# Optimization experiments

Measured on AMD Instinct MI355X. Metric: run time of the kernel, lower is better.

Reference implementation:

```python
import jax, jax.numpy as jnp
import numpy as np

N = 50000      # nodes
E = 800000     # edges (avg degree 16)
CIN = 64       # in_channels
COUT = 128     # hidden_channels (block out_channels)
TC = 512       # time_channels = 4*hidden
H = 4          # attention heads
DH = COUT // H # head dim
G = 8          # group-norm groups
SLOPE = 0.01   # LeakyReLU default slope


def group_norm(x, w, b, groups=G, eps=1e-5):
    n, c = x.shape
    xg = x.reshape(n, groups, c // groups)
    mu = xg.mean(-1, keepdims=True)
    var = xg.var(-1, keepdims=True)
    xn = ((xg - mu) * jax.lax.rsqrt(var + eps)).reshape(n, c)
    return xn * w + b


def gcn_conv(x, W, b, row, col, ew, n):
    # GCNConv: add self loops (weight 1), symmetric normalization
    sl = jnp.arange(n)
    r = jnp.concatenate([row, sl])
    c = jnp.concatenate([col, sl])
    w2 = jnp.concatenate([ew, jnp.ones((n,), ew.dtype)])
    deg = jax.ops.segment_sum(w2, c, num_segments=n)
    dinv = jnp.where(deg > 0, jax.lax.rsqrt(deg), 0.0)
    norm = dinv[r] * w2 * dinv[c]            # [E+N]
    xw = x @ W                                # [N, Cout]
    out = jax.ops.segment_sum(norm[:, None] * xw[r], c, num_segments=n)
    return out + b


def gat_conv(x, Wa, a_src, a_dst, a_edge, ba, row, col, ew, n):
    # GAT-style attention conv; self-loop edge weight filled with max(edge_weight)
    sl = jnp.arange(n)
    fill = ew.max()
    r = jnp.concatenate([row, sl])
    c = jnp.concatenate([col, sl])
    w2 = jnp.concatenate([ew, jnp.full((n,), fill, ew.dtype)])
    h = (x @ Wa).reshape(n, H, DH)            # [N, H, DH]
    al_s = (h * a_src).sum(-1)                # [N, H]
    al_d = (h * a_dst).sum(-1)                # [N, H]
    logits = jax.nn.leaky_relu(al_s[r] + al_d[c] + a_edge * w2[:, None], 0.2)
    m = jax.ops.segment_max(logits, c, num_segments=n)
    e = jnp.exp(logits - m[c])
    s = jax.ops.segment_sum(e, c, num_segments=n)
    alpha = e / (s[c] + 1e-16)                # [E+N, H]
    out = jax.ops.segment_sum(alpha[:, :, None] * h[r], c, num_segments=n)
    return out.reshape(n, H * DH) + ba


def setup_inputs() -> dict:
    key = jax.random.key(0)
    ks = jax.random.split(key, 24)
    def w(k, shape, fan_in):
        return (jax.random.normal(k, shape, jnp.float32) / np.sqrt(fan_in)).astype(jnp.float32)
    inp = {
        "x": jax.random.normal(ks[0], (N, CIN), jnp.float32),
        "t": jax.random.normal(ks[1], (TC,), jnp.float32),
        "edge_index": jax.random.randint(ks[2], (2, E), 0, N, jnp.int32),
        "edge_weight": jax.random.uniform(ks[3], (E,), jnp.float32),
        # ResBlock norm/conv params
        "gn0_w": jnp.ones((CIN,), jnp.float32), "gn0_b": jnp.zeros((CIN,), jnp.float32),
        "W1": w(ks[4], (CIN, COUT), CIN), "b1": jnp.zeros((COUT,), jnp.float32),
        "gn1_w": jnp.ones((COUT,), jnp.float32), "gn1_b": jnp.zeros((COUT,), jnp.float32),
        "W2": w(ks[5], (COUT, COUT), COUT), "b2": jnp.zeros((COUT,), jnp.float32),
        "Wres": w(ks[6], (CIN, COUT), CIN),
        "te_w": w(ks[7], (TC, COUT), TC), "te_b": jnp.zeros((COUT,), jnp.float32),
        # AttnBlock params
        "gn2_w": jnp.ones((COUT,), jnp.float32), "gn2_b": jnp.zeros((COUT,), jnp.float32),
        "Wa": w(ks[8], (COUT, H * DH), COUT),
        "a_src": w(ks[9], (H, DH), DH), "a_dst": w(ks[10], (H, DH), DH),
        "a_edge": w(ks[11], (H,), 1), "ba": jnp.zeros((H * DH,), jnp.float32),
    }
    return inp


def reference(x, t, edge_index, edge_weight,
              gn0_w, gn0_b, W1, b1, gn1_w, gn1_b, W2, b2, Wres, te_w, te_b,
              gn2_w, gn2_b, Wa, a_src, a_dst, a_edge, ba):
    row, col = edge_index[0], edge_index[1]
    leaky = lambda z: jax.nn.leaky_relu(z, SLOPE)
    # ResBlock (n_layers=2)
    h = gcn_conv(leaky(group_norm(x, gn0_w, gn0_b)), W1, b1, row, col, edge_weight, N)
    tt = leaky(t) @ te_w + te_b               # time embed, broadcasts over nodes
    h = h + tt
    h = gcn_conv(leaky(group_norm(h, gn1_w, gn1_b)), W2, b2, row, col, edge_weight, N)
    h = h + x @ Wres                          # residual (Cin != Cout -> Linear)
    # AttnBlock (n_layers=1)
    a = leaky(group_norm(h, gn2_w, gn2_b))
    out = gat_conv(a, Wa, a_src, a_dst, a_edge, ba, row, col, edge_weight, N)
    return out
```

## Files before the change

### kernel.cpp

```cpp
#include <hip/hip_runtime.h>
#include <math.h>

#define ELLW 48
#define FB 4

typedef __attribute__((ext_vector_type(8))) short frag_ab;
typedef __attribute__((ext_vector_type(4))) float frag_cd;

__device__ __forceinline__ float lk(float v, float s) { return v > 0.f ? v : v * s; }
__device__ __forceinline__ unsigned short f2b(float f) {
    unsigned u = __float_as_uint(f);
    return (unsigned short)((u + 0x7fffu + ((u >> 16) & 1u)) >> 16);
}
__device__ __forceinline__ float b2f(unsigned h) { return __uint_as_float(h << 16); }

__global__ __launch_bounds__(256) void k_init(int* cnt, float* tt,
                                              const float* __restrict__ te_b,
                                              const float* __restrict__ b1, int n) {
    int i = blockIdx.x * 256 + threadIdx.x;
    if (i < n) cnt[i] = 0;
    if (i < 128) tt[i] = te_b[i] + b1[i];
}

__global__ __launch_bounds__(256) void k_fill_ell(const int* __restrict__ row,
                                                  const int* __restrict__ col,
                                                  const float* __restrict__ ew,
                                                  int* cnt, unsigned* __restrict__ ell,
                                                  float* __restrict__ bmax, int E) {
    int base = blockIdx.x * (256 * FB);
    int tid = threadIdx.x;
    int r[FB], c[FB]; float w[FB]; bool v[FB];
#pragma unroll
    for (int i = 0; i < FB; ++i) {
        int e = base + i * 256 + tid;
        v[i] = (e < E);
        r[i] = 0; c[i] = 0; w[i] = 0.f;
        if (v[i]) { r[i] = row[e]; c[i] = col[e]; w[i] = ew[e]; }
    }
    int pos[FB];
#pragma unroll
    for (int i = 0; i < FB; ++i)
        if (v[i]) pos[i] = atomicAdd(&cnt[c[i]], 1);
#pragma unroll
    for (int i = 0; i < FB; ++i)
        if (v[i] && pos[i] < ELLW)
            ell[(size_t)c[i] * ELLW + pos[i]] = (unsigned)r[i] | ((unsigned)f2b(w[i]) << 16);
    float m = 0.f;
#pragma unroll
    for (int i = 0; i < FB; ++i) m = fmaxf(m, w[i]);
    for (int o = 32; o; o >>= 1) m = fmaxf(m, __shfl_down(m, o, 64));
    __shared__ float sm[4];
    if ((tid & 63) == 0) sm[tid >> 6] = m;
    __syncthreads();
    if (tid == 0) bmax[blockIdx.x] = fmaxf(fmaxf(sm[0], sm[1]), fmaxf(sm[2], sm[3]));
}

__global__ __launch_bounds__(256) void k_node_deg(const int* __restrict__ cnt,
                                                  const unsigned* __restrict__ ell,
                                                  float* __restrict__ dinv,
                                                  const float* __restrict__ bmax,
                                                  float* __restrict__ fill, int n, int nb) {
    int tid = threadIdx.x;
    int i = blockIdx.x * 256 + tid;
    if (i < n) {
        int c = min(cnt[i], ELLW);
        const unsigned* p = ell + (size_t)i * ELLW;
        float s = 1.f;
        for (int j = 0; j < c; ++j) s += b2f(p[j] >> 16);
        dinv[i] = rsqrtf(s);
    }
    if (blockIdx.x == 0) {
        float m = 0.f;
        for (int k = tid; k < nb; k += 256) m = fmaxf(m, bmax[k]);
        for (int o = 32; o; o >>= 1) m = fmaxf(m, __shfl_down(m, o, 64));
        __shared__ float sm[4];
        if ((tid & 63) == 0) sm[tid >> 6] = m;
        __syncthreads();
        if (tid == 0) *fill = fmaxf(fmaxf(sm[0], sm[1]), fmaxf(sm[2], sm[3]));
    }
}

__global__ __launch_bounds__(128) void k_tt(const float* __restrict__ t,
                                            const float* __restrict__ te_w, float* tt) {
    int co = threadIdx.x;
    int k0 = blockIdx.x * 32;
    float s = 0.f;
    for (int k = k0; k < k0 + 32; ++k) {
        float tv = t[k]; tv = tv > 0.f ? tv : 0.01f * tv;
        s = fmaf(tv, te_w[k * 128 + co], s);
    }
    unsafeAtomicAdd(&tt[co], s);
}

template <int K>
__device__ __forceinline__ void repack1(const float* __restrict__ W,
                                        unsigned short* __restrict__ Wp, int i) {
    int k = i >> 7, nn = i & 127;
    int kc = k >> 5, quad = (k >> 3) & 3, j = k & 7;
    Wp[(((size_t)(kc * 4 + quad) * 128) + nn) * 8 + j] = f2b(W[i]);
}

__global__ __launch_bounds__(256) void k_repack_all(const float* __restrict__ W1,
                                                    const float* __restrict__ W2,
                                                    const float* __restrict__ Wa,
                                                    const float* __restrict__ Wres,
                                                    unsigned short* W1p, unsigned short* W2p,
                                                    unsigned short* Wap, unsigned short* Wrp) {
    int i = blockIdx.x * 256 + threadIdx.x;
    if (i < 8192)        repack1<64>(W1, W1p, i);
    else if (i < 24576)  repack1<128>(W2, W2p, i - 8192);
    else if (i < 40960)  repack1<128>(Wa, Wap, i - 24576);
    else if (i < 49152)  repack1<64>(Wres, Wrp, i - 40960);
}

template <int C>
__global__ __launch_bounds__(256) void k_gn(const float* __restrict__ in,
                                            const float* __restrict__ gw,
                                            const float* __restrict__ gb,
                                            unsigned short* __restrict__ outh,
                                            unsigned short* __restrict__ rawh, int n) {
    constexpr int CPG = C / 8;
    int gid = blockIdx.x * 256 + threadIdx.x;
    int row = gid >> 3, g = gid & 7;
    if (row >= n) return;
    const float* p = in + (size_t)row * C + g * CPG;
    float v[CPG];
#pragma unroll
    for (int j = 0; j < CPG; j += 4) {
        float4 t4 = *(const float4*)(p + j);
        v[j] = t4.x; v[j + 1] = t4.y; v[j + 2] = t4.z; v[j + 3] = t4.w;
    }
    float s = 0.f, s2 = 0.f;
#pragma unroll
    for (int j = 0; j < CPG; ++j) { s += v[j]; s2 += v[j] * v[j]; }
    float mu = s * (1.0f / CPG);
    float var = s2 * (1.0f / CPG) - mu * mu;
    float rstd = rsqrtf(var + 1e-5f);
    const float* wj = gw + g * CPG;
    const float* bj = gb + g * CPG;
    unsigned pk[CPG / 2];
#pragma unroll
    for (int j = 0; j < CPG; j += 2) {
        float y0 = lk((v[j + 0] - mu) * rstd * wj[j + 0] + bj[j + 0], 0.01f);
        float y1 = lk((v[j + 1] - mu) * rstd * wj[j + 1] + bj[j + 1], 0.01f);
        pk[j / 2] = (unsigned)f2b(y0) | ((unsigned)f2b(y1) << 16);
    }
    unsigned* q = (unsigned*)(outh + (size_t)row * C + g * CPG);
#pragma unroll
    for (int j = 0; j < CPG / 2; j += 4) *(uint4*)(q + j) = *(uint4*)(pk + j);
    if (rawh) {
#pragma unroll
        for (int j = 0; j < CPG; j += 2)
            pk[j / 2] = (unsigned)f2b(v[j]) | ((unsigned)f2b(v[j + 1]) << 16);
        unsigned* q2 = (unsigned*)(rawh + (size_t)row * C + g * CPG);
#pragma unroll
        for (int j = 0; j < CPG / 2; j += 4) *(uint4*)(q2 + j) = *(uint4*)(pk + j);
    }
}

template <int K, int SCALE>
__global__ __launch_bounds__(256) void k_mgemm(const unsigned short* __restrict__ Xh,
                                               const unsigned short* __restrict__ Wp,
                                               unsigned short* __restrict__ OUTh,
                                               const float* __restrict__ dinv, int n) {
    int tid = threadIdx.x;
    int wave = tid >> 6, lane = tid & 63;
    int quad = lane >> 4, l16 = lane & 15;
    int rbase = blockIdx.x * 64 + wave * 16;
    int arow = rbase + l16; if (arow >= n) arow = n - 1;
    frag_cd acc[8];
#pragma unroll
    for (int t = 0; t < 8; ++t) acc[t] = (frag_cd){0.f, 0.f, 0.f, 0.f};
    const unsigned short* ap = Xh + (size_t)arow * K + quad * 8;
#pragma unroll
    for (int kc = 0; kc < K / 32; ++kc) {
        frag_ab a = *(const frag_ab*)(ap + kc * 32);
        const unsigned short* bp = Wp + ((size_t)(kc * 4 + quad) * 128 + l16) * 8;
#pragma unroll
        for (int t = 0; t < 8; ++t) {
            frag_ab b = *(const frag_ab*)(bp + (size_t)t * 128);
            acc[t] = __builtin_amdgcn_mfma_f32_16x16x32_bf16(a, b, acc[t], 0, 0, 0);
        }
    }
#pragma unroll
    for (int reg = 0; reg < 4; ++reg) {
        int r = rbase + quad * 4 + reg;
        if (r >= n) continue;
        float sc = 1.f;
        if constexpr (SCALE) sc = dinv[r];
#pragma unroll
        for (int t = 0; t < 8; ++t)
            OUTh[(size_t)r * 128 + t * 16 + l16] = f2b(sc * acc[t][reg]);
    }
}

__global__ __launch_bounds__(256) void k_mgemm2(const unsigned short* __restrict__ X1,
                                                const unsigned short* __restrict__ W2p,
                                                const unsigned short* __restrict__ X2,
                                                const unsigned short* __restrict__ Wrp,
                                                unsigned short* __restrict__ OUTh,
                                                float* __restrict__ C2,
                                                const float* __restrict__ bias,
                                                const float* __restrict__ dinv, int n) {
    int tid = threadIdx.x;
    int wave = tid >> 6, lane = tid & 63;
    int quad = lane >> 4, l16 = lane & 15;
    int rbase = blockIdx.x * 64 + wave * 16;
    int arow = rbase + l16; if (arow >= n) arow = n - 1;
    frag_cd acc1[8], acc2[8];
#pragma unroll
    for (int t = 0; t < 8; ++t) {
        acc1[t] = (frag_cd){0.f, 0.f, 0.f, 0.f};
        acc2[t] = (frag_cd){0.f, 0.f, 0.f, 0.f};
    }
    const unsigned short* ap1 = X1 + (size_t)arow * 128 + quad * 8;
#pragma unroll
    for (int kc = 0; kc < 4; ++kc) {
        frag_ab a = *(const frag_ab*)(ap1 + kc * 32);
        const unsigned short* bp = W2p + ((size_t)(kc * 4 + quad) * 128 + l16) * 8;
#pragma unroll
        for (int t = 0; t < 8; ++t) {
            frag_ab b = *(const frag_ab*)(bp + (size_t)t * 128);
            acc1[t] = __builtin_amdgcn_mfma_f32_16x16x32_bf16(a, b, acc1[t], 0, 0, 0);
        }
    }
    const unsigned short* ap2 = X2 + (size_t)arow * 64 + quad * 8;
#pragma unroll
    for (int kc = 0; kc < 2; ++kc) {
        frag_ab a = *(const frag_ab*)(ap2 + kc * 32);
        const unsigned short* bp = Wrp + ((size_t)(kc * 4 + quad) * 128 + l16) * 8;
#pragma unroll
        for (int t = 0; t < 8; ++t) {
            frag_ab b = *(const frag_ab*)(bp + (size_t)t * 128);
            acc2[t] = __builtin_amdgcn_mfma_f32_16x16x32_bf16(a, b, acc2[t], 0, 0, 0);
        }
    }
#pragma unroll
    for (int reg = 0; reg < 4; ++reg) {
        int r = rbase + quad * 4 + reg;
        if (r >= n) continue;
        float sc = dinv[r];
#pragma unroll
        for (int t = 0; t < 8; ++t) {
            int c = t * 16 + l16;
            size_t o = (size_t)r * 128 + c;
            OUTh[o] = f2b(sc * acc1[t][reg]);
            C2[o] = bias[c] + acc2[t][reg];
        }
    }
}

template <int BASEVEC>
__global__ __launch_bounds__(256) void k_gather_gn(const int* __restrict__ cnt,
                                                   const unsigned* __restrict__ ell,
                                                   const float* __restrict__ dinv,
                                                   const unsigned short* __restrict__ Bh,
                                                   const float* __restrict__ basevec,
                                                   const float* __restrict__ basebuf,
                                                   const float* __restrict__ gw,
                                                   const float* __restrict__ gb,
                                                   unsigned short* __restrict__ outh, int n) {
    int gid = blockIdx.x * 256 + threadIdx.x;
    int node = gid >> 5, q = gid & 31;
    if (node >= n) return;
    int s = node * ELLW;
    int e2 = s + min(cnt[node], ELLW);
    float a0 = 0.f, a1 = 0.f, a2 = 0.f, a3 = 0.f;
    int j = s;
    for (; j + 4 <= e2; j += 4) {
        uint4 pe = *(const uint4*)(ell + j);
        int r0 = pe.x & 0xffffu, r1 = pe.y & 0xffffu, r2 = pe.z & 0xffffu, r3 = pe.w & 0xffffu;
        float w0 = b2f(pe.x >> 16), w1 = b2f(pe.y >> 16);
        float w2 = b2f(pe.z >> 16), w3 = b2f(pe.w >> 16);
        uint2 v0 = *(const uint2*)(Bh + (size_t)r0 * 128 + q * 4);
        uint2 v1 = *(const uint2*)(Bh + (size_t)r1 * 128 + q * 4);
        uint2 v2 = *(const uint2*)(Bh + (size_t)r2 * 128 + q * 4);
        uint2 v3 = *(const uint2*)(Bh + (size_t)r3 * 128 + q * 4);
        a0 = fmaf(w0, b2f(v0.x & 0xffffu), a0); a1 = fmaf(w0, b2f(v0.x >> 16), a1);
        a2 = fmaf(w0, b2f(v0.y & 0xffffu), a2); a3 = fmaf(w0, b2f(v0.y >> 16), a3);
        a0 = fmaf(w1, b2f(v1.x & 0xffffu), a0); a1 = fmaf(w1, b2f(v1.x >> 16), a1);
        a2 = fmaf(w1, b2f(v1.y & 0xffffu), a2); a3 = fmaf(w1, b2f(v1.y >> 16), a3);
        a0 = fmaf(w2, b2f(v2.x & 0xffffu), a0); a1 = fmaf(w2, b2f(v2.x >> 16), a1);
        a2 = fmaf(w2, b2f(v2.y & 0xffffu), a2); a3 = fmaf(w2, b2f(v2.y >> 16), a3);
        a0 = fmaf(w3, b2f(v3.x & 0xffffu), a0); a1 = fmaf(w3, b2f(v3.x >> 16), a1);
        a2 = fmaf(w3, b2f(v3.y & 0xffffu), a2); a3 = fmaf(w3, b2f(v3.y >> 16), a3);
    }
    for (; j < e2; ++j) {
        unsigned pe = ell[j];
        int r = pe & 0xffffu;
        float nw = b2f(pe >> 16);
        uint2 hv = *(const uint2*)(Bh + (size_t)r * 128 + q * 4);
        a0 = fmaf(nw, b2f(hv.x & 0xffffu), a0);
        a1 = fmaf(nw, b2f(hv.x >> 16), a1);
        a2 = fmaf(nw, b2f(hv.y & 0xffffu), a2);
        a3 = fmaf(nw, b2f(hv.y >> 16), a3);
    }
    float dc = dinv[node];
    uint2 sv = *(const uint2*)(Bh + (size_t)node * 128 + q * 4);
    a0 = dc * (a0 + b2f(sv.x & 0xffffu));
    a1 = dc * (a1 + b2f(sv.x >> 16));
    a2 = dc * (a2 + b2f(sv.y & 0xffffu));
    a3 = dc * (a3 + b2f(sv.y >> 16));
    float h0, h1, h2, h3;
    if constexpr (BASEVEC) {
        float4 bb = *(const float4*)(basevec + q * 4);
        h0 = bb.x + a0; h1 = bb.y + a1; h2 = bb.z + a2; h3 = bb.w + a3;
    } else {
        float4 bb = *(const float4*)(basebuf + (size_t)node * 128 + q * 4);
        h0 = bb.x + a0; h1 = bb.y + a1; h2 = bb.z + a2; h3 = bb.w + a3;
    }
    float sum = (h0 + h1) + (h2 + h3);
    float sq = fmaf(h0, h0, fmaf(h1, h1, fmaf(h2, h2, h3 * h3)));
    sum += __shfl_xor(sum, 1, 64); sum += __shfl_xor(sum, 2, 64);
    sq  += __shfl_xor(sq, 1, 64);  sq  += __shfl_xor(sq, 2, 64);
    float mu = sum * (1.0f / 16.0f);
    float var = sq * (1.0f / 16.0f) - mu * mu;
    float rstd = rsqrtf(var + 1e-5f);
    float4 gwv = *(const float4*)(gw + q * 4);
    float4 gbv = *(const float4*)(gb + q * 4);
    float y0 = lk((h0 - mu) * rstd * gwv.x + gbv.x, 0.01f);
    float y1 = lk((h1 - mu) * rstd * gwv.y + gbv.y, 0.01f);
    float y2 = lk((h2 - mu) * rstd * gwv.z + gbv.z, 0.01f);
    float y3 = lk((h3 - mu) * rstd * gwv.w + gbv.w, 0.01f);
    uint2 o;
    o.x = (unsigned)f2b(y0) | ((unsigned)f2b(y1) << 16);
    o.y = (unsigned)f2b(y2) | ((unsigned)f2b(y3) << 16);
    *(uint2*)(outh + (size_t)node * 128 + q * 4) = o;
}

__global__ __launch_bounds__(256) void k_al(const unsigned short* __restrict__ HAh,
                                            const float* __restrict__ a_src,
                                            const float* __restrict__ a_dst,
                                            float* __restrict__ als, float* __restrict__ ald, int n) {
    int gid = blockIdx.x * 256 + threadIdx.x;
    if (gid >= n * 4) return;
    int row = gid >> 2, hd = gid & 3;
    const unsigned* p = (const unsigned*)(HAh + (size_t)row * 128 + hd * 32);
    float ss = 0.f, sd = 0.f;
#pragma unroll
    for (int j = 0; j < 16; ++j) {
        unsigned u = p[j];
        float f0 = b2f(u & 0xffffu), f1 = b2f(u >> 16);
        float s0 = a_src[hd * 32 + j * 2], s1 = a_src[hd * 32 + j * 2 + 1];
        float d0 = a_dst[hd * 32 + j * 2], d1 = a_dst[hd * 32 + j * 2 + 1];
        ss = fmaf(f0, s0, fmaf(f1, s1, ss));
        sd = fmaf(f0, d0, fmaf(f1, d1, sd));
    }
    als[gid] = ss; ald[gid] = sd;
}

__global__ __launch_bounds__(256) void k_gat_gather(const int* __restrict__ cnt,
                                                    const unsigned* __restrict__ ell,
                                                    const float* __restrict__ als,
                                                    const float* __restrict__ ald,
                                                    const float* __restrict__ a_edge,
                                                    const float* __restrict__ fill,
                                                    const unsigned short* __restrict__ HAh,
                                                    const float* __restrict__ ba,
                                                    float* __restrict__ out, int n) {
    int gid = blockIdx.x * 256 + threadIdx.x;
    int node = gid >> 5, q = gid & 31, hd = q >> 3;
    if (node >= n) return;
    int s = node * ELLW;
    int e2 = s + min(cnt[node], ELLW);
    float ae = a_edge[hd];
    float aldc = ald[node * 4 + hd];
    float wself = *fill;
    float pself = __expf(lk(als[node * 4 + hd] + aldc + ae * wself, 0.2f));
    float den = pself;
    uint2 hv = *(const uint2*)(HAh + (size_t)node * 128 + q * 4);
    float a0 = pself * b2f(hv.x & 0xffffu), a1 = pself * b2f(hv.x >> 16);
    float a2 = pself * b2f(hv.y & 0xffffu), a3 = pself * b2f(hv.y >> 16);
    int j = s;
    for (; j + 4 <= e2; j += 4) {
        uint4 pe = *(const uint4*)(ell + j);
        int r0 = pe.x & 0xffffu, r1 = pe.y & 0xffffu, r2 = pe.z & 0xffffu, r3 = pe.w & 0xffffu;
        float w0 = b2f(pe.x >> 16), w1 = b2f(pe.y >> 16);
        float w2 = b2f(pe.z >> 16), w3 = b2f(pe.w >> 16);
        float s0 = als[r0 * 4 + hd], s1 = als[r1 * 4 + hd];
        float s2 = als[r2 * 4 + hd], s3 = als[r3 * 4 + hd];
        uint2 v0 = *(const uint2*)(HAh + (size_t)r0 * 128 + q * 4);
        uint2 v1 = *(const uint2*)(HAh + (size_t)r1 * 128 + q * 4);
        uint2 v2 = *(const uint2*)(HAh + (size_t)r2 * 128 + q * 4);
        uint2 v3 = *(const uint2*)(HAh + (size_t)r3 * 128 + q * 4);
        float pe0 = __expf(lk(s0 + aldc + ae * w0, 0.2f));
        float pe1 = __expf(lk(s1 + aldc + ae * w1, 0.2f));
        float pe2 = __expf(lk(s2 + aldc + ae * w2, 0.2f));
        float pe3 = __expf(lk(s3 + aldc + ae * w3, 0.2f));
        den += (pe0 + pe1) + (pe2 + pe3);
        a0 = fmaf(pe0, b2f(v0.x & 0xffffu), a0); a1 = fmaf(pe0, b2f(v0.x >> 16), a1);
        a2 = fmaf(pe0, b2f(v0.y & 0xffffu), a2); a3 = fmaf(pe0, b2f(v0.y >> 16), a3);
        a0 = fmaf(pe1, b2f(v1.x & 0xffffu), a0); a1 = fmaf(pe1, b2f(v1.x >> 16), a1);
        a2 = fmaf(pe1, b2f(v1.y & 0xffffu), a2); a3 = fmaf(pe1, b2f(v1.y >> 16), a3);
        a0 = fmaf(pe2, b2f(v2.x & 0xffffu), a0); a1 = fmaf(pe2, b2f(v2.x >> 16), a1);
        a2 = fmaf(pe2, b2f(v2.y & 0xffffu), a2); a3 = fmaf(pe2, b2f(v2.y >> 16), a3);
        a0 = fmaf(pe3, b2f(v3.x & 0xffffu), a0); a1 = fmaf(pe3, b2f(v3.x >> 16), a1);
        a2 = fmaf(pe3, b2f(v3.y & 0xffffu), a2); a3 = fmaf(pe3, b2f(v3.y >> 16), a3);
    }
    for (; j < e2; ++j) {
        unsigned pe = ell[j];
        int r = pe & 0xffffu;
        float w = b2f(pe >> 16);
        float pev = __expf(lk(als[r * 4 + hd] + aldc + ae * w, 0.2f));
        den += pev;
        uint2 v = *(const uint2*)(HAh + (size_t)r * 128 + q * 4);
        a0 = fmaf(pev, b2f(v.x & 0xffffu), a0);
        a1 = fmaf(pev, b2f(v.x >> 16), a1);
        a2 = fmaf(pev, b2f(v.y & 0xffffu), a2);
        a3 = fmaf(pev, b2f(v.y >> 16), a3);
    }
    float inv = 1.0f / (den + 1e-16f);
    const float* bb = ba + q * 4;
    float4 o;
    o.x = bb[0] + a0 * inv; o.y = bb[1] + a1 * inv;
    o.z = bb[2] + a2 * inv; o.w = bb[3] + a3 * inv;
    *(float4*)&out[(size_t)node * 128 + q * 4] = o;
}

extern "C" void kernel_launch(void* const* d_in, const int* in_sizes, int n_in,
                              void* d_out, int out_size, void* d_ws, size_t ws_size,
                              hipStream_t stream) {
    const float* x     = (const float*)d_in[0];
    const float* t     = (const float*)d_in[1];
    const int*   eidx  = (const int*)d_in[2];
    const float* ew    = (const float*)d_in[3];
    const float* gn0_w = (const float*)d_in[4];
    const float* gn0_b = (const float*)d_in[5];
    const float* W1    = (const float*)d_in[6];
    const float* b1    = (const float*)d_in[7];
    const float* gn1_w = (const float*)d_in[8];
    const float* gn1_b = (const float*)d_in[9];
    const float* W2    = (const float*)d_in[10];
    const float* b2    = (const float*)d_in[11];
    const float* Wres  = (const float*)d_in[12];
    const float* te_w  = (const float*)d_in[13];
    const float* te_b  = (const float*)d_in[14];
    const float* gn2_w = (const float*)d_in[15];
    const float* gn2_b = (const float*)d_in[16];
    const float* Wa    = (const float*)d_in[17];
    const float* a_src = (const float*)d_in[18];
    const float* a_dst = (const float*)d_in[19];
    const float* a_edge= (const float*)d_in[20];
    const float* ba    = (const float*)d_in[21];

    int n = in_sizes[0] / 64;
    int E = in_sizes[3];
    const int* rowp = eidx;
    const int* colp = eidx + E;

    char* p = (char*)d_ws;
    float* fC = (float*)p;                 p += (size_t)n * 128 * 4;
    unsigned short* fDh = (unsigned short*)p; p += (size_t)n * 128 * 2;
    unsigned short* fBh = (unsigned short*)p; p += (size_t)n * 128 * 2;
    unsigned short* xh  = (unsigned short*)p; p += (size_t)n * 64 * 2;
    unsigned* ell = (unsigned*)p;          p += (size_t)n * ELLW * 4;
    unsigned short* W1p   = (unsigned short*)p; p += 64 * 128 * 2;
    unsigned short* W2p   = (unsigned short*)p; p += 128 * 128 * 2;
    unsigned short* Wap   = (unsigned short*)p; p += 128 * 128 * 2;
    unsigned short* Wresp = (unsigned short*)p; p += 64 * 128 * 2;
    float* dinv = (float*)p;               p += (size_t)n * 4;
    float* tt  = (float*)p;                p += 128 * 4;
    float* fill = (float*)p;               p += 16;
    float* als = (float*)p;                p += (size_t)4 * n * 4;
    float* ald = (float*)p;                p += (size_t)4 * n * 4;
    int* cnt    = (int*)p;                 p += (size_t)n * 4;
    float* bmax = (float*)p;               p += 4096 * 4;
    float* out = (float*)d_out;

    auto cdiv = [](long long a, long long b) { return (int)((a + b - 1) / b); };
    int nbf = cdiv(E, 256 * FB);

    k_init<<<cdiv(n, 256), 256, 0, stream>>>(cnt, tt, te_b, b1, n);
    k_fill_ell<<<nbf, 256, 0, stream>>>(rowp, colp, ew, cnt, ell, bmax, E);
    k_node_deg<<<cdiv(n, 256), 256, 0, stream>>>(cnt, ell, dinv, bmax, fill, n, nbf);
    k_tt<<<16, 128, 0, stream>>>(t, te_w, tt);
    k_repack_all<<<cdiv(49152, 256), 256, 0, stream>>>(W1, W2, Wa, Wres, W1p, W2p, Wap, Wresp);

    k_gn<64><<<cdiv(8LL * n, 256), 256, 0, stream>>>(x, gn0_w, gn0_b, fDh, xh, n);
    k_mgemm<64, 1><<<cdiv(n, 64), 256, 0, stream>>>(fDh, W1p, fBh, dinv, n);
    k_gather_gn<1><<<cdiv(32LL * n, 256), 256, 0, stream>>>(cnt, ell, dinv, fBh, tt, nullptr,
                                                            gn1_w, gn1_b, fDh, n);

    k_mgemm2<<<cdiv(n, 64), 256, 0, stream>>>(fDh, W2p, xh, Wresp, fBh, fC, b2, dinv, n);
    k_gather_gn<0><<<cdiv(32LL * n, 256), 256, 0, stream>>>(cnt, ell, dinv, fBh, nullptr, fC,
                                                            gn2_w, gn2_b, fDh, n);

    k_mgemm<128, 0><<<cdiv(n, 64), 256, 0, stream>>>(fDh, Wap, fBh, nullptr, n);
    k_al<<<cdiv(4LL * n, 256), 256, 0, stream>>>(fBh, a_src, a_dst, als, ald, n);
    k_gat_gather<<<cdiv(32LL * n, 256), 256, 0, stream>>>(cnt, ell, als, ald, a_edge, fill, fBh, ba, out, n);
}
```

Before: 326.3 us.

## Build ELL via bucketed counting sort and fuse group-norm and attention logits into GEMMs

Replaces the per-edge global atomic ELL fill with a two-level bucketed counting sort: a block histogram over 256-node buckets, a scan, a scatter into a staging buffer, then a per-bucket shared-memory build that also writes counts and inverse degrees. It also fuses the first group-norm into the first MFMA GEMM, computes the attention source/destination logits inside the attention GEMM epilogue from fp32 accumulators, and merges the time embedding, fill reduction and weight repacking into one prep kernel. The aim is to cut global atomic contention, scattered writes and launch count, at the cost of extra passes over the edges and a staging buffer of E*8 bytes. Edge order within a node can now differ, which changes floating-point summation order.

```diff
diff --git a/kernel.cpp b/kernel.cpp
--- a/kernel.cpp
+++ b/kernel.cpp
@@ -2,7 +2,7 @@
 #include <math.h>
 
 #define ELLW 48
-#define FB 4
+#define CH 4096
 
 typedef __attribute__((ext_vector_type(8))) short frag_ab;
 typedef __attribute__((ext_vector_type(4))) float frag_cd;
@@ -14,40 +14,79 @@
 }
 __device__ __forceinline__ float b2f(unsigned h) { return __uint_as_float(h << 16); }
 
-__global__ __launch_bounds__(256) void k_init(int* cnt, float* tt,
-                                              const float* __restrict__ te_b,
-                                              const float* __restrict__ b1, int n) {
-    int i = blockIdx.x * 256 + threadIdx.x;
-    if (i < n) cnt[i] = 0;
-    if (i < 128) tt[i] = te_b[i] + b1[i];
-}
-
-__global__ __launch_bounds__(256) void k_fill_ell(const int* __restrict__ row,
+__global__ __launch_bounds__(256) void k_bhist(const int* __restrict__ col,
+                                               int* __restrict__ bhist, int E, int NB) {
+    __shared__ int lh[256];
+    int tid = threadIdx.x;
+    if (tid < NB) lh[tid] = 0;
+    __syncthreads();
+    int base = blockIdx.x * CH;
+#pragma unroll
+    for (int i = 0; i < CH / 256; ++i) {
+        int e = base + i * 256 + tid;
+        if (e < E) atomicAdd(&lh[col[e] >> 8], 1);
+    }
+    __syncthreads();
+    if (tid < NB && lh[tid]) atomicAdd(&bhist[tid], lh[tid]);
+}
+
+__global__ __launch_bounds__(256) void k_bscan(const int* __restrict__ bhist,
+                                               int* __restrict__ boff,
+                                               int* __restrict__ cursor, int NB, int E) {
+    __shared__ int s[256];
+    int tid = threadIdx.x;
+    int v = (tid < NB) ? bhist[tid] : 0;
+    s[tid] = v; __syncthreads();
+#pragma unroll
+    for (int d = 1; d < 256; d <<= 1) {
+        int t = (tid >= d) ? s[tid - d] : 0;
+        __syncthreads();
+        s[tid] += t;
+        __syncthreads();
+    }
+    if (tid < NB) { int o = s[tid] - v; boff[tid] = o; cursor[tid] = o; }
+    if (tid == 0) boff[NB] = E;
+}
+
+__global__ __launch_bounds__(256) void k_bscatter(const int* __restrict__ row,
                                                   const int* __restrict__ col,
                                                   const float* __restrict__ ew,
-                                                  int* cnt, unsigned* __restrict__ ell,
-                                                  float* __restrict__ bmax, int E) {
-    int base = blockIdx.x * (256 * FB);
-    int tid = threadIdx.x;
-    int r[FB], c[FB]; float w[FB]; bool v[FB];
-#pragma unroll
-    for (int i = 0; i < FB; ++i) {
+                                                  int* __restrict__ cursor,
+                                                  uint2* __restrict__ stage,
+                                                  float* __restrict__ bmax, int E, int NB) {
+    __shared__ int lh[256];
+    __shared__ int lbase[256];
+    constexpr int PT = CH / 256;
+    int tid = threadIdx.x;
+    if (tid < NB) lh[tid] = 0;
+    __syncthreads();
+    int base = blockIdx.x * CH;
+    unsigned entry[PT]; int cc[PT]; int lpos[PT]; bool val[PT];
+    float m = 0.f;
+#pragma unroll
+    for (int i = 0; i < PT; ++i) {
         int e = base + i * 256 + tid;
-        v[i] = (e < E);
-        r[i] = 0; c[i] = 0; w[i] = 0.f;
-        if (v[i]) { r[i] = row[e]; c[i] = col[e]; w[i] = ew[e]; }
-    }
-    int pos[FB];
-#pragma unroll
-    for (int i = 0; i < FB; ++i)
-        if (v[i]) pos[i] = atomicAdd(&cnt[c[i]], 1);
-#pragma unroll
-    for (int i = 0; i < FB; ++i)
-        if (v[i] && pos[i] < ELLW)
-            ell[(size_t)c[i] * ELLW + pos[i]] = (unsigned)r[i] | ((unsigned)f2b(w[i]) << 16);
-    float m = 0.f;
-#pragma unroll
-    for (int i = 0; i < FB; ++i) m = fmaxf(m, w[i]);
+        val[i] = (e < E);
+        entry[i] = 0; cc[i] = 0; lpos[i] = 0;
+        if (val[i]) {
+            int r = row[e], c = col[e];
+            float w = ew[e];
+            m = fmaxf(m, w);
+            entry[i] = (unsigned)r | ((unsigned)f2b(w) << 16);
+            cc[i] = c;
+            lpos[i] = atomicAdd(&lh[c >> 8], 1);
+        }
+    }
+    __syncthreads();
+    if (tid < NB) lbase[tid] = lh[tid] ? atomicAdd(&cursor[tid], lh[tid]) : 0;
+    __syncthreads();
+#pragma unroll
+    for (int i = 0; i < PT; ++i) {
+        if (val[i]) {
+            int b = cc[i] >> 8;
+            stage[lbase[b] + lpos[i]] = make_uint2(entry[i], (unsigned)(cc[i] & 255));
+        }
+    }
     for (int o = 32; o; o >>= 1) m = fmaxf(m, __shfl_down(m, o, 64));
     __shared__ float sm[4];
     if ((tid & 63) == 0) sm[tid >> 6] = m;
@@ -55,41 +94,36 @@
     if (tid == 0) bmax[blockIdx.x] = fmaxf(fmaxf(sm[0], sm[1]), fmaxf(sm[2], sm[3]));
 }
 
-__global__ __launch_bounds__(256) void k_node_deg(const int* __restrict__ cnt,
-                                                  const unsigned* __restrict__ ell,
-                                                  float* __restrict__ dinv,
-                                                  const float* __restrict__ bmax,
-                                                  float* __restrict__ fill, int n, int nb) {
-    int tid = threadIdx.x;
-    int i = blockIdx.x * 256 + tid;
-    if (i < n) {
-        int c = min(cnt[i], ELLW);
-        const unsigned* p = ell + (size_t)i * ELLW;
-        float s = 1.f;
-        for (int j = 0; j < c; ++j) s += b2f(p[j] >> 16);
-        dinv[i] = rsqrtf(s);
-    }
-    if (blockIdx.x == 0) {
-        float m = 0.f;
-        for (int k = tid; k < nb; k += 256) m = fmaxf(m, bmax[k]);
-        for (int o = 32; o; o >>= 1) m = fmaxf(m, __shfl_down(m, o, 64));
-        __shared__ float sm[4];
-        if ((tid & 63) == 0) sm[tid >> 6] = m;
-        __syncthreads();
-        if (tid == 0) *fill = fmaxf(fmaxf(sm[0], sm[1]), fmaxf(sm[2], sm[3]));
-    }
-}
-
-__global__ __launch_bounds__(128) void k_tt(const float* __restrict__ t,
-                                            const float* __restrict__ te_w, float* tt) {
-    int co = threadIdx.x;
-    int k0 = blockIdx.x * 32;
-    float s = 0.f;
-    for (int k = k0; k < k0 + 32; ++k) {
-        float tv = t[k]; tv = tv > 0.f ? tv : 0.01f * tv;
-        s = fmaf(tv, te_w[k * 128 + co], s);
-    }
-    unsafeAtomicAdd(&tt[co], s);
+__global__ __launch_bounds__(256) void k_bbuild(const int* __restrict__ boff,
+                                                const uint2* __restrict__ stage,
+                                                unsigned* __restrict__ ell,
+                                                int* __restrict__ cnt,
+                                                float* __restrict__ dinv, int n) {
+    __shared__ unsigned tile[256 * ELLW];
+    __shared__ int lcnt[256];
+    int tid = threadIdx.x;
+    int bk = blockIdx.x;
+    lcnt[tid] = 0;
+    __syncthreads();
+    int s = boff[bk], e2 = boff[bk + 1];
+    for (int i = s + tid; i < e2; i += 256) {
+        uint2 p = stage[i];
+        int c8 = p.y;
+        int pos = atomicAdd(&lcnt[c8], 1);
+        if (pos < ELLW) tile[c8 * ELLW + pos] = p.x;
+    }
+    __syncthreads();
+    int node = bk * 256 + tid;
+    if (node >= n) return;
+    int c = min(lcnt[tid], ELLW);
+    cnt[node] = c;
+    float sw = 1.f;
+    for (int j = 0; j < c; ++j) sw += b2f(tile[tid * ELLW + j] >> 16);
+    dinv[node] = rsqrtf(sw);
+    unsigned* dst = ell + (size_t)node * ELLW;
+#pragma unroll
+    for (int j = 0; j < ELLW / 4; ++j)
+        *(uint4*)(dst + j * 4) = *(uint4*)(tile + tid * ELLW + j * 4);
 }
 
 template <int K>
@@ -100,94 +134,102 @@
     Wp[(((size_t)(kc * 4 + quad) * 128) + nn) * 8 + j] = f2b(W[i]);
 }
 
-__global__ __launch_bounds__(256) void k_repack_all(const float* __restrict__ W1,
-                                                    const float* __restrict__ W2,
-                                                    const float* __restrict__ Wa,
-                                                    const float* __restrict__ Wres,
-                                                    unsigned short* W1p, unsigned short* W2p,
-                                                    unsigned short* Wap, unsigned short* Wrp) {
-    int i = blockIdx.x * 256 + threadIdx.x;
-    if (i < 8192)        repack1<64>(W1, W1p, i);
-    else if (i < 24576)  repack1<128>(W2, W2p, i - 8192);
-    else if (i < 40960)  repack1<128>(Wa, Wap, i - 24576);
-    else if (i < 49152)  repack1<64>(Wres, Wrp, i - 40960);
-}
-
-template <int C>
-__global__ __launch_bounds__(256) void k_gn(const float* __restrict__ in,
-                                            const float* __restrict__ gw,
-                                            const float* __restrict__ gb,
-                                            unsigned short* __restrict__ outh,
-                                            unsigned short* __restrict__ rawh, int n) {
-    constexpr int CPG = C / 8;
-    int gid = blockIdx.x * 256 + threadIdx.x;
-    int row = gid >> 3, g = gid & 7;
-    if (row >= n) return;
-    const float* p = in + (size_t)row * C + g * CPG;
-    float v[CPG];
-#pragma unroll
-    for (int j = 0; j < CPG; j += 4) {
-        float4 t4 = *(const float4*)(p + j);
-        v[j] = t4.x; v[j + 1] = t4.y; v[j + 2] = t4.z; v[j + 3] = t4.w;
-    }
-    float s = 0.f, s2 = 0.f;
-#pragma unroll
-    for (int j = 0; j < CPG; ++j) { s += v[j]; s2 += v[j] * v[j]; }
-    float mu = s * (1.0f / CPG);
-    float var = s2 * (1.0f / CPG) - mu * mu;
-    float rstd = rsqrtf(var + 1e-5f);
-    const float* wj = gw + g * CPG;
-    const float* bj = gb + g * CPG;
-    unsigned pk[CPG / 2];
-#pragma unroll
-    for (int j = 0; j < CPG; j += 2) {
-        float y0 = lk((v[j + 0] - mu) * rstd * wj[j + 0] + bj[j + 0], 0.01f);
-        float y1 = lk((v[j + 1] - mu) * rstd * wj[j + 1] + bj[j + 1], 0.01f);
-        pk[j / 2] = (unsigned)f2b(y0) | ((unsigned)f2b(y1) << 16);
-    }
-    unsigned* q = (unsigned*)(outh + (size_t)row * C + g * CPG);
-#pragma unroll
-    for (int j = 0; j < CPG / 2; j += 4) *(uint4*)(q + j) = *(uint4*)(pk + j);
-    if (rawh) {
-#pragma unroll
-        for (int j = 0; j < CPG; j += 2)
-            pk[j / 2] = (unsigned)f2b(v[j]) | ((unsigned)f2b(v[j + 1]) << 16);
-        unsigned* q2 = (unsigned*)(rawh + (size_t)row * C + g * CPG);
-#pragma unroll
-        for (int j = 0; j < CPG / 2; j += 4) *(uint4*)(q2 + j) = *(uint4*)(pk + j);
-    }
-}
-
-template <int K, int SCALE>
-__global__ __launch_bounds__(256) void k_mgemm(const unsigned short* __restrict__ Xh,
-                                               const unsigned short* __restrict__ Wp,
-                                               unsigned short* __restrict__ OUTh,
-                                               const float* __restrict__ dinv, int n) {
+__global__ __launch_bounds__(256) void k_prep(const float* __restrict__ t,
+                                              const float* __restrict__ te_w,
+                                              const float* __restrict__ te_b,
+                                              const float* __restrict__ b1,
+                                              float* __restrict__ tt,
+                                              const float* __restrict__ bmax,
+                                              float* __restrict__ fill, int nbm,
+                                              const float* __restrict__ W1,
+                                              const float* __restrict__ W2,
+                                              const float* __restrict__ Wa,
+                                              const float* __restrict__ Wres,
+                                              unsigned short* W1p, unsigned short* W2p,
+                                              unsigned short* Wap, unsigned short* Wrp) {
+    int tid = threadIdx.x;
+    int blk = blockIdx.x;
+    if (blk == 0) {
+        if (tid < 128) {
+            float s = te_b[tid] + b1[tid];
+            for (int k = 0; k < 512; ++k) {
+                float tv = t[k]; tv = tv > 0.f ? tv : 0.01f * tv;
+                s = fmaf(tv, te_w[k * 128 + tid], s);
+            }
+            tt[tid] = s;
+        }
+    } else if (blk == 1) {
+        float m = 0.f;
+        for (int i = tid; i < nbm; i += 256) m = fmaxf(m, bmax[i]);
+        for (int o = 32; o; o >>= 1) m = fmaxf(m, __shfl_down(m, o, 64));
+        __shared__ float sm[4];
+        if ((tid & 63) == 0) sm[tid >> 6] = m;
+        __syncthreads();
+        if (tid == 0) *fill = fmaxf(fmaxf(sm[0], sm[1]), fmaxf(sm[2], sm[3]));
+    } else {
+        int i = (blk - 2) * 256 + tid;
+        if (i < 8192)        repack1<64>(W1, W1p, i);
+        else if (i < 24576)  repack1<128>(W2, W2p, i - 8192);
+        else if (i < 40960)  repack1<128>(Wa, Wap, i - 24576);
+        else if (i < 49152)  repack1<64>(Wres, Wrp, i - 40960);
+    }
+}
+
+__global__ __launch_bounds__(256) void k_mgemm1(const float* __restrict__ X,
+                                                const float* __restrict__ gw,
+                                                const float* __restrict__ gb,
+                                                const unsigned short* __restrict__ Wp,
+                                                unsigned short* __restrict__ OUTh,
+                                                unsigned short* __restrict__ xh,
+                                                const float* __restrict__ dinv, int n) {
     int tid = threadIdx.x;
     int wave = tid >> 6, lane = tid & 63;
     int quad = lane >> 4, l16 = lane & 15;
     int rbase = blockIdx.x * 64 + wave * 16;
     int arow = rbase + l16; if (arow >= n) arow = n - 1;
+    frag_ab afrag[2];
+    const float* xr = X + (size_t)arow * 64 + quad * 8;
+#pragma unroll
+    for (int kc = 0; kc < 2; ++kc) {
+        float4 u0 = *(const float4*)(xr + kc * 32);
+        float4 u1 = *(const float4*)(xr + kc * 32 + 4);
+        float v[8] = {u0.x, u0.y, u0.z, u0.w, u1.x, u1.y, u1.z, u1.w};
+        float s = 0.f, sq = 0.f;
+#pragma unroll
+        for (int j = 0; j < 8; ++j) { s += v[j]; sq = fmaf(v[j], v[j], sq); }
+        float mu = s * 0.125f;
+        float var = sq * 0.125f - mu * mu;
+        float rstd = rsqrtf(var + 1e-5f);
+        const float* wj = gw + kc * 32 + quad * 8;
+        const float* bj = gb + kc * 32 + quad * 8;
+        unsigned pk[4], pr[4];
+#pragma unroll
+        for (int j = 0; j < 8; j += 2) {
+            float y0 = lk((v[j + 0] - mu) * rstd * wj[j + 0] + bj[j + 0], 0.01f);
+            float y1 = lk((v[j + 1] - mu) * rstd * wj[j + 1] + bj[j + 1], 0.01f);
+            pk[j / 2] = (unsigned)f2b(y0) | ((unsigned)f2b(y1) << 16);
+            pr[j / 2] = (unsigned)f2b(v[j]) | ((unsigned)f2b(v[j + 1]) << 16);
+        }
+        afrag[kc] = *(frag_ab*)pk;
+        *(uint4*)(xh + (size_t)arow * 64 + kc * 32 + quad * 8) = *(uint4*)pr;
+    }
     frag_cd acc[8];
 #pragma unroll
     for (int t = 0; t < 8; ++t) acc[t] = (frag_cd){0.f, 0.f, 0.f, 0.f};
-    const unsigned short* ap = Xh + (size_t)arow * K + quad * 8;
-#pragma unroll
-    for (int kc = 0; kc < K / 32; ++kc) {
-        frag_ab a = *(const frag_ab*)(ap + kc * 32);
+#pragma unroll
+    for (int kc = 0; kc < 2; ++kc) {
         const unsigned short* bp = Wp + ((size_t)(kc * 4 + quad) * 128 + l16) * 8;
 #pragma unroll
         for (int t = 0; t < 8; ++t) {
             frag_ab b = *(const frag_ab*)(bp + (size_t)t * 128);
-            acc[t] = __builtin_amdgcn_mfma_f32_16x16x32_bf16(a, b, acc[t], 0, 0, 0);
+            acc[t] = __builtin_amdgcn_mfma_f32_16x16x32_bf16(afrag[kc], b, acc[t], 0, 0, 0);
         }
     }
 #pragma unroll
     for (int reg = 0; reg < 4; ++reg) {
         int r = rbase + quad * 4 + reg;
         if (r >= n) continue;
-        float sc = 1.f;
-        if constexpr (SCALE) sc = dinv[r];
+        float sc = dinv[r];
 #pragma unroll
         for (int t = 0; t < 8; ++t)
             OUTh[(size_t)r * 128 + t * 16 + l16] = f2b(sc * acc[t][reg]);
@@ -246,6 +288,75 @@
             size_t o = (size_t)r * 128 + c;
             OUTh[o] = f2b(sc * acc1[t][reg]);
             C2[o] = bias[c] + acc2[t][reg];
+        }
+    }
+}
+
+__global__ __launch_bounds__(256) void k_mgemmA(const unsigned short* __restrict__ Xh,
+                                                const unsigned short* __restrict__ Wp,
+                                                unsigned short* __restrict__ OUTh,
+                                                const float* __restrict__ a_src,
+                                                const float* __restrict__ a_dst,
+                                                float* __restrict__ als,
+                                                float* __restrict__ ald, int n) {
+    int tid = threadIdx.x;
+    int wave = tid >> 6, lane = tid & 63;
+    int quad = lane >> 4, l16 = lane & 15;
+    int rbase = blockIdx.x * 64 + wave * 16;
+    int arow = rbase + l16; if (arow >= n) arow = n - 1;
+    frag_cd acc[8];
+#pragma unroll
+    for (int t = 0; t < 8; ++t) acc[t] = (frag_cd){0.f, 0.f, 0.f, 0.f};
+    const unsigned short* ap = Xh + (size_t)arow * 128 + quad * 8;
+#pragma unroll
+    for (int kc = 0; kc < 4; ++kc) {
+        frag_ab a = *(const frag_ab*)(ap + kc * 32);
+        const unsigned short* bp = Wp + ((size_t)(kc * 4 + quad) * 128 + l16) * 8;
+#pragma unroll
+        for (int t = 0; t < 8; ++t) {
+            frag_ab b = *(const frag_ab*)(bp + (size_t)t * 128);
+            acc[t] = __builtin_amdgcn_mfma_f32_16x16x32_bf16(a, b, acc[t], 0, 0, 0);
+        }
+    }
+#pragma unroll
+    for (int reg = 0; reg < 4; ++reg) {
+        int r = rbase + quad * 4 + reg;
+        if (r >= n) continue;
+#pragma unroll
+        for (int t = 0; t < 8; ++t)
+            OUTh[(size_t)r * 128 + t * 16 + l16] = f2b(acc[t][reg]);
+    }
+    float ps[4][4], pd[4][4];
+#pragma unroll
+    for (int hd = 0; hd < 4; ++hd) {
+        float slo = a_src[hd * 32 + l16], shi = a_src[hd * 32 + 16 + l16];
+        float dlo = a_dst[hd * 32 + l16], dhi = a_dst[hd * 32 + 16 + l16];
+#pragma unroll
+        for (int reg = 0; reg < 4; ++reg) {
+            ps[reg][hd] = fmaf(acc[2 * hd][reg], slo, acc[2 * hd + 1][reg] * shi);
+            pd[reg][hd] = fmaf(acc[2 * hd][reg], dlo, acc[2 * hd + 1][reg] * dhi);
+        }
+    }
+#pragma unroll
+    for (int m = 1; m < 16; m <<= 1) {
+#pragma unroll
+        for (int reg = 0; reg < 4; ++reg)
+#pragma unroll
+            for (int hd = 0; hd < 4; ++hd) {
+                ps[reg][hd] += __shfl_xor(ps[reg][hd], m, 64);
+                pd[reg][hd] += __shfl_xor(pd[reg][hd], m, 64);
+            }
+    }
+    if (l16 == 0) {
+#pragma unroll
+        for (int reg = 0; reg < 4; ++reg) {
+            int r = rbase + quad * 4 + reg;
+            if (r >= n) continue;
+#pragma unroll
+            for (int hd = 0; hd < 4; ++hd) {
+                als[r * 4 + hd] = ps[reg][hd];
+                ald[r * 4 + hd] = pd[reg][hd];
+            }
         }
     }
 }
@@ -326,27 +437,6 @@
     o.x = (unsigned)f2b(y0) | ((unsigned)f2b(y1) << 16);
     o.y = (unsigned)f2b(y2) | ((unsigned)f2b(y3) << 16);
     *(uint2*)(outh + (size_t)node * 128 + q * 4) = o;
-}
-
-__global__ __launch_bounds__(256) void k_al(const unsigned short* __restrict__ HAh,
-                                            const float* __restrict__ a_src,
-                                            const float* __restrict__ a_dst,
-                                            float* __restrict__ als, float* __restrict__ ald, int n) {
-    int gid = blockIdx.x * 256 + threadIdx.x;
-    if (gid >= n * 4) return;
-    int row = gid >> 2, hd = gid & 3;
-    const unsigned* p = (const unsigned*)(HAh + (size_t)row * 128 + hd * 32);
-    float ss = 0.f, sd = 0.f;
-#pragma unroll
-    for (int j = 0; j < 16; ++j) {
-        unsigned u = p[j];
-        float f0 = b2f(u & 0xffffu), f1 = b2f(u >> 16);
-        float s0 = a_src[hd * 32 + j * 2], s1 = a_src[hd * 32 + j * 2 + 1];
-        float d0 = a_dst[hd * 32 + j * 2], d1 = a_dst[hd * 32 + j * 2 + 1];
-        ss = fmaf(f0, s0, fmaf(f1, s1, ss));
-        sd = fmaf(f0, d0, fmaf(f1, d1, sd));
-    }
-    als[gid] = ss; ald[gid] = sd;
 }
 
 __global__ __launch_bounds__(256) void k_gat_gather(const int* __restrict__ cnt,
@@ -447,6 +537,7 @@
     int E = in_sizes[3];
     const int* rowp = eidx;
     const int* colp = eidx + E;
+    int NB = (n + 255) >> 8;
 
     char* p = (char*)d_ws;
     float* fC = (float*)p;                 p += (size_t)n * 128 * 4;
@@ -454,6 +545,7 @@
     unsigned short* fBh = (unsigned short*)p; p += (size_t)n * 128 * 2;
     unsigned short* xh  = (unsigned short*)p; p += (size_t)n * 64 * 2;
     unsigned* ell = (unsigned*)p;          p += (size_t)n * ELLW * 4;
+    uint2* stage = (uint2*)p;              p += (size_t)E * 8;
     unsigned short* W1p   = (unsigned short*)p; p += 64 * 128 * 2;
     unsigned short* W2p   = (unsigned short*)p; p += 128 * 128 * 2;
     unsigned short* Wap   = (unsigned short*)p; p += 128 * 128 * 2;
@@ -464,20 +556,24 @@
     float* als = (float*)p;                p += (size_t)4 * n * 4;
     float* ald = (float*)p;                p += (size_t)4 * n * 4;
     int* cnt    = (int*)p;                 p += (size_t)n * 4;
+    int* bhist  = (int*)p;                 p += 256 * 4;
+    int* boff   = (int*)p;                 p += 260 * 4;
+    int* cursor = (int*)p;                 p += 256 * 4;
     float* bmax = (float*)p;               p += 4096 * 4;
     float* out = (float*)d_out;
 
     auto cdiv = [](long long a, long long b) { return (int)((a + b - 1) / b); };
-    int nbf = cdiv(E, 256 * FB);
-
-    k_init<<<cdiv(n, 256), 256, 0, stream>>>(cnt, tt, te_b, b1, n);
-    k_fill_ell<<<nbf, 256, 0, stream>>>(rowp, colp, ew, cnt, ell, bmax, E);
-    k_node_deg<<<cdiv(n, 256), 256, 0, stream>>>(cnt, ell, dinv, bmax, fill, n, nbf);
-    k_tt<<<16, 128, 0, stream>>>(t, te_w, tt);
-    k_repack_all<<<cdiv(49152, 256), 256, 0, stream>>>(W1, W2, Wa, Wres, W1p, W2p, Wap, Wresp);
-
-    k_gn<64><<<cdiv(8LL * n, 256), 256, 0, stream>>>(x, gn0_w, gn0_b, fDh, xh, n);
-    k_mgemm<64, 1><<<cdiv(n, 64), 256, 0, stream>>>(fDh, W1p, fBh, dinv, n);
+    int gridE = cdiv(E, CH);
+
+    hipMemsetAsync(bhist, 0, NB * 4, stream);
+    k_bhist<<<gridE, 256, 0, stream>>>(colp, bhist, E, NB);
+    k_bscan<<<1, 256, 0, stream>>>(bhist, boff, cursor, NB, E);
+    k_bscatter<<<gridE, 256, 0, stream>>>(rowp, colp, ew, cursor, stage, bmax, E, NB);
+    k_bbuild<<<NB, 256, 0, stream>>>(boff, stage, ell, cnt, dinv, n);
+    k_prep<<<194, 256, 0, stream>>>(t, te_w, te_b, b1, tt, bmax, fill, gridE,
+                                    W1, W2, Wa, Wres, W1p, W2p, Wap, Wresp);
+
+    k_mgemm1<<<cdiv(n, 64), 256, 0, stream>>>(x, gn0_w, gn0_b, W1p, fBh, xh, dinv, n);
     k_gather_gn<1><<<cdiv(32LL * n, 256), 256, 0, stream>>>(cnt, ell, dinv, fBh, tt, nullptr,
                                                             gn1_w, gn1_b, fDh, n);
 
@@ -485,7 +581,6 @@
     k_gather_gn<0><<<cdiv(32LL * n, 256), 256, 0, stream>>>(cnt, ell, dinv, fBh, nullptr, fC,
                                                             gn2_w, gn2_b, fDh, n);
 
-    k_mgemm<128, 0><<<cdiv(n, 64), 256, 0, stream>>>(fDh, Wap, fBh, nullptr, n);
-    k_al<<<cdiv(4LL * n, 256), 256, 0, stream>>>(fBh, a_src, a_dst, als, ald, n);
+    k_mgemmA<<<cdiv(n, 64), 256, 0, stream>>>(fDh, Wap, fBh, a_src, a_dst, als, ald, n);
     k_gat_gather<<<cdiv(32LL * n, 256), 256, 0, stream>>>(cnt, ell, als, ald, a_edge, fill, fBh, ba, out, n);
 }
```

Result: no change. 322.7 us (-1.1%).
